# Kernel tuning notes

Hardware: AMD Instinct MI355X
Metric: run time of the kernel (lower is better)

Reference implementation:

```python
import jax, jax.numpy as jnp
import numpy as np

B, T, C = 2, 2048, 1024
H = 4 * C           # MLP hidden (4*n_embd)
E_DYN = 7           # num_experts - static_experts
TOP_K = 2           # num_experts_per_tok
MOE_LOSS_COEF = 0.01


def setup_inputs() -> dict:
    key = jax.random.key(0)
    ks = jax.random.split(key, 6)
    s = 0.02
    x = jax.random.normal(ks[0], (B, T, C), dtype=jnp.float32)
    gate_w = jax.random.normal(ks[1], (C, E_DYN), dtype=jnp.float32) * s
    w1 = jax.random.normal(ks[2], (E_DYN, C, H), dtype=jnp.float32) * s   # dynamic experts c_fc
    w2 = jax.random.normal(ks[3], (E_DYN, H, C), dtype=jnp.float32) * s   # dynamic experts c_proj
    w1s = jax.random.normal(ks[4], (C, H), dtype=jnp.float32) * s         # static expert c_fc
    w2s = jax.random.normal(ks[5], (H, C), dtype=jnp.float32) * s         # static expert c_proj
    return {"x": x, "gate_w": gate_w, "w1": w1, "w2": w2, "w1s": w1s, "w2s": w2s}


def reference(x, gate_w, w1, w2, w1s, w2s):
    b, t, c = x.shape
    xf = x.reshape(-1, c)                                   # [N, C]
    n = xf.shape[0]

    # static expert (always applied)
    y_static = jax.nn.gelu(xf @ w1s, approximate=False) @ w2s  # [N, C]

    # gating: top-k + softmax over selected scores
    scores = xf @ gate_w                                    # [N, E]
    topk_scores, topk_idx = jax.lax.top_k(scores, TOP_K)    # [N, K]
    topk_w = jax.nn.softmax(topk_scores, axis=-1)           # [N, K]

    # dense dispatch weights [N, E] (top_k indices are distinct -> set is safe)
    probs = jnp.zeros((n, E_DYN), dtype=x.dtype)
    probs = probs.at[jnp.arange(n)[:, None], topk_idx].set(topk_w)

    # all-expert MLP then weighted combine (same math as masked per-expert dispatch)
    h = jax.nn.gelu(jnp.einsum('nc,ech->enh', xf, w1), approximate=False)  # [E, N, H]
    y_all = jnp.einsum('enh,ehc->enc', h, w2)               # [E, N, C]
    y_dyn = jnp.einsum('ne,enc->nc', probs, y_all)          # [N, C]

    y = (y_dyn + y_static).reshape(b, t, c)

    # variance_penalty auxiliary loss
    expert_usage = probs.mean(axis=0)                       # [E]
    variance = jnp.mean((expert_usage - expert_usage.mean()) ** 2)
    aux = MOE_LOSS_COEF * variance
    return y, aux
```

## Files before the change

kernel.cpp:

```cpp
#include <hip/hip_runtime.h>
#include <hip/hip_bf16.h>
#include <math.h>

#define N_TOK 4096
#define C_DIM 1024
#define H_DIM 4096
#define NEXP 7
#define NGRP 8
#define HCAP 13184

typedef __attribute__((ext_vector_type(8))) short short8;
typedef __attribute__((ext_vector_type(4))) float floatx4;

static const size_t OFF_COUNTS = 0;
static const size_t OFF_CURSOR = 64;
static const size_t OFF_BASE   = 128;
static const size_t OFF_PCOUNT = 192;
static const size_t OFF_CNT8   = 256;
static const size_t OFF_USAGE  = 320;
static const size_t OFF_TOPKI  = 4096;
static const size_t OFF_TOPKW  = OFF_TOPKI + 8192ull * 4;
static const size_t OFF_ETOK   = OFF_TOPKW + 8192ull * 4;
static const size_t OFF_EWT    = OFF_ETOK + (size_t)HCAP * 4;
static const size_t OFF_EIDX   = OFF_EWT + (size_t)HCAP * 4;
static const size_t OFF_XB     = 262144;
static const size_t OFF_W1T    = OFF_XB + (size_t)N_TOK * C_DIM * 2;
static const size_t OFF_W2T    = OFF_W1T + (size_t)NGRP * H_DIM * C_DIM * 2;
static const size_t OFF_H      = OFF_W2T + (size_t)NGRP * C_DIM * H_DIM * 2;

static __device__ __forceinline__ unsigned short f2bf(float f) {
    __hip_bfloat16 b = __float2bfloat16(f);
    return *reinterpret_cast<unsigned short*>(&b);
}
static __device__ __forceinline__ float bf2f(unsigned short u) {
    unsigned int v = ((unsigned int)u) << 16;
    return __builtin_bit_cast(float, v);
}

static __device__ __forceinline__ float gelu_f(float v) {
    float z = v * 0.70710678118654752f;
    float az = fabsf(z);
    float t = 1.0f / (1.0f + 0.3275911f * az);
    float poly = t * (0.254829592f + t * (-0.284496736f + t * (1.421413741f +
                 t * (-1.453152027f + t * 1.061405429f))));
    float erf_abs = 1.0f - poly * __expf(-az * az);
    float erf_v = (z < 0.f) ? -erf_abs : erf_abs;
    return 0.5f * v * (1.0f + erf_v);
}

static __device__ __forceinline__ void gll16(const void* g, void* l) {
    __builtin_amdgcn_global_load_lds((const __attribute__((address_space(1))) void*)g,
                                     (__attribute__((address_space(3))) void*)l, 16, 0, 0);
}

static __device__ __forceinline__ void wait_vm8() { asm volatile("s_waitcnt vmcnt(8)" ::: "memory"); }
static __device__ __forceinline__ void wait_vm4() { asm volatile("s_waitcnt vmcnt(4)" ::: "memory"); }
static __device__ __forceinline__ void wait_vm0() { asm volatile("s_waitcnt vmcnt(0)" ::: "memory"); }
static __device__ __forceinline__ void barf() {
    __builtin_amdgcn_s_barrier();
    asm volatile("" ::: "memory");
}

__global__ void init_small_kernel(int* counts, int* cursor, float* usage) {
    int i = threadIdx.x;
    if (i < 8) { counts[i] = 0; cursor[i] = 0; usage[i] = 0.f; }
}

__global__ void convert_x_kernel(const float* __restrict__ x, unsigned short* __restrict__ xb) {
    int i = blockIdx.x * 256 + threadIdx.x;
    float4 v = ((const float4*)x)[i];
    ushort4 o;
    o.x = f2bf(v.x); o.y = f2bf(v.y); o.z = f2bf(v.z); o.w = f2bf(v.w);
    ((ushort4*)xb)[i] = o;
}

__global__ __launch_bounds__(256) void transpose_cvt_kernel(
    const float* __restrict__ dyn, const float* __restrict__ stat,
    __hip_bfloat16* __restrict__ dst, int R, int S)
{
    int e = blockIdx.z;
    const float* src = (e < NEXP) ? (dyn + (size_t)e * R * S) : stat;
    unsigned short* d = (unsigned short*)(dst + (size_t)e * R * S);
    int s0 = blockIdx.x * 32, r0 = blockIdx.y * 64;
    __shared__ float t[64][33];
    int tx4 = threadIdx.x & 15, ty4 = threadIdx.x >> 4;
#pragma unroll
    for (int i = 0; i < 4; i++) {
        int r = ty4 + i * 16;
        float2 v = *(const float2*)(src + (size_t)(r0 + r) * S + s0 + tx4 * 2);
        t[r][tx4 * 2] = v.x; t[r][tx4 * 2 + 1] = v.y;
    }
    __syncthreads();
    int tx3 = threadIdx.x & 31, ty3 = threadIdx.x >> 5;
#pragma unroll
    for (int i = 0; i < 4; i++) {
        int s = ty3 + i * 8;
        int r = tx3 * 2;
        ushort2 o;
        o.x = f2bf(t[r][s]); o.y = f2bf(t[r + 1][s]);
        *(ushort2*)(d + (size_t)(s0 + s) * R + r0 + r) = o;
    }
}

__global__ __launch_bounds__(256) void gate_kernel(
    const float* __restrict__ x, const float* __restrict__ gw,
    int* __restrict__ topki, float* __restrict__ topkw,
    int* counts, float* usage)
{
    int wid = threadIdx.x >> 6, lane = threadIdx.x & 63;
    int t = blockIdx.x * 4 + wid;
    float s[NEXP];
#pragma unroll
    for (int e = 0; e < NEXP; e++) s[e] = 0.f;
    for (int c = lane; c < C_DIM; c += 64) {
        float xv = x[(size_t)t * C_DIM + c];
#pragma unroll
        for (int e = 0; e < NEXP; e++) s[e] += xv * gw[c * NEXP + e];
    }
#pragma unroll
    for (int e = 0; e < NEXP; e++)
        for (int off = 32; off > 0; off >>= 1) s[e] += __shfl_xor(s[e], off);
    if (lane == 0) {
        int e0 = 0;
        for (int e = 1; e < NEXP; e++) if (s[e] > s[e0]) e0 = e;
        int e1 = -1;
        for (int e = 0; e < NEXP; e++) {
            if (e == e0) continue;
            if (e1 < 0 || s[e] > s[e1]) e1 = e;
        }
        float w0 = 1.f / (1.f + expf(s[e1] - s[e0]));
        float w1 = 1.f - w0;
        topki[t * 2] = e0; topki[t * 2 + 1] = e1;
        topkw[t * 2] = w0; topkw[t * 2 + 1] = w1;
        atomicAdd(&counts[e0], 1); atomicAdd(&counts[e1], 1);
        atomicAdd(&usage[e0], w0); atomicAdd(&usage[e1], w1);
    }
}

__global__ __launch_bounds__(256) void prefix_kernel(
    const int* counts, const float* usage,
    int* base, int* pcount, int* cnt8,
    int* etok, float* ewt, float* y, int aux_index)
{
    __shared__ int sb[NGRP], sc[NGRP], sp[NGRP];
    if (threadIdx.x == 0) {
        int run = 0;
        for (int g = 0; g < NEXP; g++) {
            int c = counts[g];
            int p = (c + 127) & ~127;
            base[g] = run; pcount[g] = p; cnt8[g] = c;
            sb[g] = run; sc[g] = c; sp[g] = p;
            run += p;
        }
        base[NEXP] = run; pcount[NEXP] = N_TOK; cnt8[NEXP] = N_TOK;
        sb[NEXP] = run; sc[NEXP] = N_TOK; sp[NEXP] = N_TOK;
        float u[NEXP]; float mean = 0.f;
        for (int e = 0; e < NEXP; e++) { u[e] = usage[e] / (float)N_TOK; mean += u[e]; }
        mean /= (float)NEXP;
        float var = 0.f;
        for (int e = 0; e < NEXP; e++) { float dd = u[e] - mean; var += dd * dd; }
        var /= (float)NEXP;
        y[aux_index] = 0.01f * var;
    }
    __syncthreads();
    for (int i = threadIdx.x; i < N_TOK; i += 256) {
        etok[sb[NEXP] + i] = i; ewt[sb[NEXP] + i] = 1.0f;
    }
    for (int g = 0; g < NEXP; g++) {
        for (int i = sc[g] + (int)threadIdx.x; i < sp[g]; i += 256) {
            etok[sb[g] + i] = 0; ewt[sb[g] + i] = 0.f;
        }
    }
}

__global__ void scatter_kernel(const int* __restrict__ topki, const float* __restrict__ topkw,
                               const int* __restrict__ base, int* cursor,
                               int* __restrict__ etok, float* __restrict__ ewt,
                               int* __restrict__ eidx)
{
    int i = blockIdx.x * 256 + threadIdx.x;
    int t = i >> 1;
    int e = topki[i];
    float w = topkw[i];
    int pos = atomicAdd(&cursor[e], 1);
    int idx = base[e] + pos;
    etok[idx] = t; ewt[idx] = w;
    eidx[i] = idx;
}


#define STG1(T) do { int b_ = (T) & 3; size_t so_ = (size_t)(T) * 64; \
        gll16(pA0 + so_, &Als[b_][w * 1024]); \
        gll16(pA1 + so_, &Als[b_][8192 + w * 1024]); \
        gll16(pB0 + so_, &Bls[b_][w * 1024]); \
        gll16(pB1 + so_, &Bls[b_][8192 + w * 1024]); } while (0)

__global__ __launch_bounds__(512, 2) void gemm1_kernel(
    const __hip_bfloat16* __restrict__ xb,
    const __hip_bfloat16* __restrict__ w1t,
    __hip_bfloat16* __restrict__ h,
    const int* __restrict__ etok,
    const int* __restrict__ base,
    const int* __restrict__ pcount)
{
    int id = blockIdx.x;
    int xcd = id & 7, rest = id >> 3;
    int ct = rest & 15, s = rest >> 4;
    int g = s & 7;
    int mt = ((xcd - g) & 7) + 8 * (s >> 3);
    int psz = pcount[g];
    if (mt * 256 >= psz) return;
    int eb = base[g];

    __shared__ __align__(16) char Als[4][16384];
    __shared__ __align__(16) char Bls[4][16384];

    int tid = threadIdx.x, lane = tid & 63, w = tid >> 6;
    int r0 = tid >> 2, c0 = tid & 3;
    int cs = c0 ^ ((r0 >> 1) & 3);

    int tokA0 = etok[eb + mt * 256 + r0];
    int tokA1 = etok[eb + mt * 256 + 128 + r0];
    const char* pA0 = (const char*)(xb + (size_t)tokA0 * C_DIM) + cs * 16;
    const char* pA1 = (const char*)(xb + (size_t)tokA1 * C_DIM) + cs * 16;
    const char* pB0 = (const char*)(w1t + ((size_t)g * H_DIM + ct * 256 + r0) * C_DIM) + cs * 16;
    const char* pB1 = (const char*)(w1t + ((size_t)g * H_DIM + ct * 256 + 128 + r0) * C_DIM) + cs * 16;

    int wm = w >> 2, wn = w & 3;
    int quad = lane >> 4, l16 = lane & 15;
    int rswz = (quad ^ ((l16 >> 1) & 3)) * 16;

    floatx4 acc[8][4] = {};
    const int NT = C_DIM / 32;
    STG1(0); STG1(1); STG1(2);
    for (int T = 0; T < NT; ++T) {
        int rem = NT - 1 - T;
        if (rem >= 2) wait_vm8(); else if (rem == 1) wait_vm4(); else wait_vm0();
        barf();
        if (T + 3 < NT) STG1(T + 3);
        const char* Ap = Als[T & 3];
        const char* Bp = Bls[T & 3];
        short8 a[8], b[4];
#pragma unroll
        for (int i = 0; i < 8; i++)
            a[i] = *(const short8*)(Ap + (wm * 128 + i * 16 + l16) * 64 + rswz);
#pragma unroll
        for (int j = 0; j < 4; j++)
            b[j] = *(const short8*)(Bp + (wn * 64 + j * 16 + l16) * 64 + rswz);
        __builtin_amdgcn_s_setprio(1);
#pragma unroll
        for (int i = 0; i < 8; i++)
#pragma unroll
            for (int j = 0; j < 4; j++)
                acc[i][j] = __builtin_amdgcn_mfma_f32_16x16x32_bf16(a[i], b[j], acc[i][j], 0, 0, 0);
        __builtin_amdgcn_s_setprio(0);
    }

#pragma unroll
    for (int i = 0; i < 8; i++) {
        int lr0 = mt * 256 + wm * 128 + i * 16 + quad * 4;
#pragma unroll
        for (int reg = 0; reg < 4; reg++) {
            int lr = lr0 + reg;
            if (lr < psz) {
                size_t hrow = (size_t)(eb + lr) * H_DIM;
#pragma unroll
                for (int j = 0; j < 4; j++) {
                    int cc = ct * 256 + wn * 64 + j * 16 + l16;
                    h[hrow + cc] = __float2bfloat16(gelu_f(acc[i][j][reg]));
                }
            }
        }
    }
}

__global__ __launch_bounds__(512, 2) void gemm2_kernel(
    const __hip_bfloat16* __restrict__ h,
    const __hip_bfloat16* __restrict__ w2t,
    unsigned short* __restrict__ yp,
    const int* __restrict__ base,
    const int* __restrict__ pcount)
{
    int id = blockIdx.x;
    int xcd = id & 7, rest = id >> 3;
    int ct = rest & 3, s = rest >> 2;
    int g = s & 7;
    int mt = ((xcd - g) & 7) + 8 * (s >> 3);
    int psz = pcount[g];
    if (mt * 256 >= psz) return;
    int eb = base[g];

    __shared__ __align__(16) char Als[4][16384];
    __shared__ __align__(16) char Bls[4][16384];

    int tid = threadIdx.x, lane = tid & 63, w = tid >> 6;
    int r0 = tid >> 2, c0 = tid & 3;
    int cs = c0 ^ ((r0 >> 1) & 3);

    const char* pA0 = (const char*)(h + (size_t)(eb + mt * 256 + r0) * H_DIM) + cs * 16;
    const char* pA1 = (const char*)(h + (size_t)(eb + mt * 256 + 128 + r0) * H_DIM) + cs * 16;
    const char* pB0 = (const char*)(w2t + ((size_t)g * C_DIM + ct * 256 + r0) * H_DIM) + cs * 16;
    const char* pB1 = (const char*)(w2t + ((size_t)g * C_DIM + ct * 256 + 128 + r0) * H_DIM) + cs * 16;

    int wm = w >> 2, wn = w & 3;
    int quad = lane >> 4, l16 = lane & 15;
    int rswz = (quad ^ ((l16 >> 1) & 3)) * 16;

    floatx4 acc[8][4] = {};
    const int NT = H_DIM / 32;
    STG1(0); STG1(1); STG1(2);
    for (int T = 0; T < NT; ++T) {
        int rem = NT - 1 - T;
        if (rem >= 2) wait_vm8(); else if (rem == 1) wait_vm4(); else wait_vm0();
        barf();
        if (T + 3 < NT) STG1(T + 3);
        const char* Ap = Als[T & 3];
        const char* Bp = Bls[T & 3];
        short8 a[8], b[4];
#pragma unroll
        for (int i = 0; i < 8; i++)
            a[i] = *(const short8*)(Ap + (wm * 128 + i * 16 + l16) * 64 + rswz);
#pragma unroll
        for (int j = 0; j < 4; j++)
            b[j] = *(const short8*)(Bp + (wn * 64 + j * 16 + l16) * 64 + rswz);
        __builtin_amdgcn_s_setprio(1);
#pragma unroll
        for (int i = 0; i < 8; i++)
#pragma unroll
            for (int j = 0; j < 4; j++)
                acc[i][j] = __builtin_amdgcn_mfma_f32_16x16x32_bf16(a[i], b[j], acc[i][j], 0, 0, 0);
        __builtin_amdgcn_s_setprio(0);
    }

#pragma unroll
    for (int i = 0; i < 8; i++) {
        int lr0 = mt * 256 + wm * 128 + i * 16 + quad * 4;
#pragma unroll
        for (int reg = 0; reg < 4; reg++) {
            int lr = lr0 + reg;
            if (lr < psz) {
                size_t yrow = (size_t)(eb + lr) * C_DIM;
#pragma unroll
                for (int j = 0; j < 4; j++) {
                    int cc = ct * 256 + wn * 64 + j * 16 + l16;
                    yp[yrow + cc] = f2bf(acc[i][j][reg]);
                }
            }
        }
    }
}

__global__ __launch_bounds__(256) void combine_kernel(
    const unsigned short* __restrict__ yp,
    const int* __restrict__ eidx,
    const float* __restrict__ topkw,
    const int* __restrict__ base,
    float* __restrict__ y)
{
    int t = blockIdx.x;
    int i0 = eidx[t * 2], i1 = eidx[t * 2 + 1];
    float w0 = topkw[t * 2], w1 = topkw[t * 2 + 1];
    int is = base[NEXP] + t;
    int c = threadIdx.x * 4;
    ushort4 a = *(const ushort4*)(yp + (size_t)i0 * C_DIM + c);
    ushort4 b = *(const ushort4*)(yp + (size_t)i1 * C_DIM + c);
    ushort4 s = *(const ushort4*)(yp + (size_t)is * C_DIM + c);
    float4 o;
    o.x = w0 * bf2f(a.x) + w1 * bf2f(b.x) + bf2f(s.x);
    o.y = w0 * bf2f(a.y) + w1 * bf2f(b.y) + bf2f(s.y);
    o.z = w0 * bf2f(a.z) + w1 * bf2f(b.z) + bf2f(s.z);
    o.w = w0 * bf2f(a.w) + w1 * bf2f(b.w) + bf2f(s.w);
    *(float4*)(y + (size_t)t * C_DIM + c) = o;
}

extern "C" void kernel_launch(void* const* d_in, const int* in_sizes, int n_in,
                              void* d_out, int out_size, void* d_ws, size_t ws_size,
                              hipStream_t stream) {
    const float* x      = (const float*)d_in[0];
    const float* gate_w = (const float*)d_in[1];
    const float* w1     = (const float*)d_in[2];
    const float* w2     = (const float*)d_in[3];
    const float* w1s    = (const float*)d_in[4];
    const float* w2s    = (const float*)d_in[5];
    float* y = (float*)d_out;
    char* ws = (char*)d_ws;

    int*   counts = (int*)(ws + OFF_COUNTS);
    int*   cursor = (int*)(ws + OFF_CURSOR);
    int*   base   = (int*)(ws + OFF_BASE);
    int*   pcount = (int*)(ws + OFF_PCOUNT);
    int*   cnt8   = (int*)(ws + OFF_CNT8);
    float* usage  = (float*)(ws + OFF_USAGE);
    int*   topki  = (int*)(ws + OFF_TOPKI);
    float* topkw  = (float*)(ws + OFF_TOPKW);
    int*   etok   = (int*)(ws + OFF_ETOK);
    float* ewt    = (float*)(ws + OFF_EWT);
    int*   eidx   = (int*)(ws + OFF_EIDX);
    unsigned short* xb_u = (unsigned short*)(ws + OFF_XB);
    __hip_bfloat16* xb  = (__hip_bfloat16*)(ws + OFF_XB);
    __hip_bfloat16* w1t = (__hip_bfloat16*)(ws + OFF_W1T);
    __hip_bfloat16* w2t = (__hip_bfloat16*)(ws + OFF_W2T);
    __hip_bfloat16* hbuf = (__hip_bfloat16*)(ws + OFF_H);
    unsigned short* yp  = (unsigned short*)(ws + OFF_W1T);

    init_small_kernel<<<1, 64, 0, stream>>>(counts, cursor, usage);

    convert_x_kernel<<<(N_TOK * C_DIM / 4) / 256, 256, 0, stream>>>(x, xb_u);
    transpose_cvt_kernel<<<dim3(H_DIM / 32, C_DIM / 64, NGRP), 256, 0, stream>>>(w1, w1s, w1t, C_DIM, H_DIM);
    transpose_cvt_kernel<<<dim3(C_DIM / 32, H_DIM / 64, NGRP), 256, 0, stream>>>(w2, w2s, w2t, H_DIM, C_DIM);

    gate_kernel<<<N_TOK / 4, 256, 0, stream>>>(x, gate_w, topki, topkw, counts, usage);
    prefix_kernel<<<1, 256, 0, stream>>>(counts, usage, base, pcount, cnt8, etok, ewt, y, N_TOK * C_DIM);
    scatter_kernel<<<(N_TOK * 2) / 256, 256, 0, stream>>>(topki, topkw, base, cursor, etok, ewt, eidx);

    gemm1_kernel<<<4096, 512, 0, stream>>>(xb, w1t, hbuf, etok, base, pcount);
    gemm2_kernel<<<1024, 512, 0, stream>>>(hbuf, w2t, yp, base, pcount);
    combine_kernel<<<N_TOK, 256, 0, stream>>>(yp, eidx, topkw, base, y);
}
```

Measured before the change: 856.6 us.

## Rewrite grouped GEMM main loop with K=64 double-buffered ping-pong schedule

Replaces the per-K32 four-stage GEMM loop in both expert GEMMs with a shared core that stages K=64 tiles into 128KB of double-buffered LDS. It splits each tile into four quarter MFMA phases with interleaved LDS reads and global-to-LDS prefetches, separated by barriers. It also fuses the x-to-bf16 conversion into the gate kernel and widens the weight transpose tiles to 64x64 with float4 loads. The aim is to hide global latency behind MFMA work and cut kernel launches and memory passes. The cost is more barriers per iteration and a large LDS footprint that may limit occupancy under launch_bounds(512,2).

```diff
diff --git a/kernel.cpp b/kernel.cpp
--- a/kernel.cpp
+++ b/kernel.cpp
@@ -53,27 +53,20 @@
                                      (__attribute__((address_space(3))) void*)l, 16, 0, 0);
 }
 
-static __device__ __forceinline__ void wait_vm8() { asm volatile("s_waitcnt vmcnt(8)" ::: "memory"); }
-static __device__ __forceinline__ void wait_vm4() { asm volatile("s_waitcnt vmcnt(4)" ::: "memory"); }
-static __device__ __forceinline__ void wait_vm0() { asm volatile("s_waitcnt vmcnt(0)" ::: "memory"); }
 static __device__ __forceinline__ void barf() {
     __builtin_amdgcn_s_barrier();
     asm volatile("" ::: "memory");
 }
+static __device__ __forceinline__ void lgkm0s() {
+    asm volatile("s_waitcnt lgkmcnt(0)" ::: "memory");
+    __builtin_amdgcn_sched_barrier(0);
+}
 
 __global__ void init_small_kernel(int* counts, int* cursor, float* usage) {
     int i = threadIdx.x;
     if (i < 8) { counts[i] = 0; cursor[i] = 0; usage[i] = 0.f; }
 }
 
-__global__ void convert_x_kernel(const float* __restrict__ x, unsigned short* __restrict__ xb) {
-    int i = blockIdx.x * 256 + threadIdx.x;
-    float4 v = ((const float4*)x)[i];
-    ushort4 o;
-    o.x = f2bf(v.x); o.y = f2bf(v.y); o.z = f2bf(v.z); o.w = f2bf(v.w);
-    ((ushort4*)xb)[i] = o;
-}
-
 __global__ __launch_bounds__(256) void transpose_cvt_kernel(
     const float* __restrict__ dyn, const float* __restrict__ stat,
     __hip_bfloat16* __restrict__ dst, int R, int S)
@@ -81,29 +74,29 @@
     int e = blockIdx.z;
     const float* src = (e < NEXP) ? (dyn + (size_t)e * R * S) : stat;
     unsigned short* d = (unsigned short*)(dst + (size_t)e * R * S);
-    int s0 = blockIdx.x * 32, r0 = blockIdx.y * 64;
-    __shared__ float t[64][33];
-    int tx4 = threadIdx.x & 15, ty4 = threadIdx.x >> 4;
+    int s0 = blockIdx.x * 64, r0 = blockIdx.y * 64;
+    __shared__ float t[64][65];
+    int lx = (threadIdx.x & 15) * 4, ty = threadIdx.x >> 4;
 #pragma unroll
     for (int i = 0; i < 4; i++) {
-        int r = ty4 + i * 16;
-        float2 v = *(const float2*)(src + (size_t)(r0 + r) * S + s0 + tx4 * 2);
-        t[r][tx4 * 2] = v.x; t[r][tx4 * 2 + 1] = v.y;
+        int r = ty + i * 16;
+        float4 v = *(const float4*)(src + (size_t)(r0 + r) * S + s0 + lx);
+        t[r][lx] = v.x; t[r][lx + 1] = v.y; t[r][lx + 2] = v.z; t[r][lx + 3] = v.w;
     }
     __syncthreads();
-    int tx3 = threadIdx.x & 31, ty3 = threadIdx.x >> 5;
 #pragma unroll
     for (int i = 0; i < 4; i++) {
-        int s = ty3 + i * 8;
-        int r = tx3 * 2;
-        ushort2 o;
-        o.x = f2bf(t[r][s]); o.y = f2bf(t[r + 1][s]);
-        *(ushort2*)(d + (size_t)(s0 + s) * R + r0 + r) = o;
+        int ss = ty + i * 16;
+        ushort4 o;
+        o.x = f2bf(t[lx][ss]); o.y = f2bf(t[lx + 1][ss]);
+        o.z = f2bf(t[lx + 2][ss]); o.w = f2bf(t[lx + 3][ss]);
+        *(ushort4*)(d + (size_t)(s0 + ss) * R + r0 + lx) = o;
     }
 }
 
 __global__ __launch_bounds__(256) void gate_kernel(
     const float* __restrict__ x, const float* __restrict__ gw,
+    unsigned short* __restrict__ xb,
     int* __restrict__ topki, float* __restrict__ topkw,
     int* counts, float* usage)
 {
@@ -112,10 +105,22 @@
     float s[NEXP];
 #pragma unroll
     for (int e = 0; e < NEXP; e++) s[e] = 0.f;
-    for (int c = lane; c < C_DIM; c += 64) {
-        float xv = x[(size_t)t * C_DIM + c];
-#pragma unroll
-        for (int e = 0; e < NEXP; e++) s[e] += xv * gw[c * NEXP + e];
+#pragma unroll
+    for (int it = 0; it < 4; ++it) {
+        int c = it * 256 + lane * 4;
+        float4 xv = *(const float4*)(x + (size_t)t * C_DIM + c);
+        ushort4 o;
+        o.x = f2bf(xv.x); o.y = f2bf(xv.y); o.z = f2bf(xv.z); o.w = f2bf(xv.w);
+        *(ushort4*)(xb + (size_t)t * C_DIM + c) = o;
+        const float* g0 = gw + (size_t)c * NEXP;
+#pragma unroll
+        for (int e = 0; e < NEXP; e++) s[e] += xv.x * g0[e];
+#pragma unroll
+        for (int e = 0; e < NEXP; e++) s[e] += xv.y * g0[NEXP + e];
+#pragma unroll
+        for (int e = 0; e < NEXP; e++) s[e] += xv.z * g0[2 * NEXP + e];
+#pragma unroll
+        for (int e = 0; e < NEXP; e++) s[e] += xv.w * g0[3 * NEXP + e];
     }
 #pragma unroll
     for (int e = 0; e < NEXP; e++)
@@ -189,11 +194,91 @@
 }
 
 
-#define STG1(T) do { int b_ = (T) & 3; size_t so_ = (size_t)(T) * 64; \
-        gll16(pA0 + so_, &Als[b_][w * 1024]); \
-        gll16(pA1 + so_, &Als[b_][8192 + w * 1024]); \
-        gll16(pB0 + so_, &Bls[b_][w * 1024]); \
-        gll16(pB1 + so_, &Bls[b_][8192 + w * 1024]); } while (0)
+static __device__ __forceinline__ void mfma16(const short8 (&a)[8], const short8 (&b)[4],
+                                              floatx4 (&acc)[8][4], int mo, int no) {
+#pragma unroll
+    for (int i = 0; i < 4; i++)
+#pragma unroll
+        for (int j = 0; j < 2; j++)
+#pragma unroll
+            for (int kk = 0; kk < 2; kk++)
+                acc[mo + i][no + j] = __builtin_amdgcn_mfma_f32_16x16x32_bf16(
+                    a[i * 2 + kk], b[j * 2 + kk], acc[mo + i][no + j], 0, 0, 0);
+}
+static __device__ __forceinline__ void rdA(short8 (&d)[8], const char* b, int sw0, int sw1) {
+#pragma unroll
+    for (int i = 0; i < 4; i++) {
+        d[i * 2]     = *(const short8*)(b + i * 2048 + sw0);
+        d[i * 2 + 1] = *(const short8*)(b + i * 2048 + sw1);
+    }
+}
+static __device__ __forceinline__ void rdB(short8 (&d)[4], const char* b, int sw0, int sw1) {
+#pragma unroll
+    for (int j = 0; j < 2; j++) {
+        d[j * 2]     = *(const short8*)(b + j * 2048 + sw0);
+        d[j * 2 + 1] = *(const short8*)(b + j * 2048 + sw1);
+    }
+}
+
+static __device__ __forceinline__ void gemm_core(char* lds, int NKT,
+    const char* pA0, const char* pA1, const char* pA2, const char* pA3,
+    const char* pB0, const char* pB1, const char* pB2, const char* pB3,
+    floatx4 (&acc)[8][4])
+{
+    int tid = threadIdx.x, lane = tid & 63, w = tid >> 6;
+    int wm = w >> 2, wn = w & 3, l16 = lane & 15, quad = lane >> 4;
+    int sw0 = ((quad ^ (l16 & 7)) << 4);
+    int sw1 = (((4 + quad) ^ (l16 & 7)) << 4);
+    int aoff = (wm * 64 + l16) * 128;
+    int boff = (wn * 32 + l16) * 128;
+    int wb = w * 1024;
+    short8 aM0[8], aM1[8], bN0[4], bN1[4];
+
+#define SA_(h, doff, ko) do { \
+    gll16(((h) ? pA1 : pA0) + (ko), lds + (doff) + (h) * 16384 + wb); \
+    gll16(((h) ? pA3 : pA2) + (ko), lds + (doff) + (h) * 16384 + 8192 + wb); } while (0)
+#define SB_(nh, doff, ko) do { \
+    gll16(((nh) ? pB1 : pB0) + (ko), lds + 65536 + (doff) + (nh) * 16384 + wb); \
+    gll16(((nh) ? pB3 : pB2) + (ko), lds + 65536 + (doff) + (nh) * 16384 + 8192 + wb); } while (0)
+
+    SA_(0, 0, 0); SA_(1, 0, 0); SB_(0, 0, 0); SB_(1, 0, 0);
+    SA_(0, 32768, 128); SA_(1, 32768, 128); SB_(0, 32768, 128);
+    asm volatile("s_waitcnt vmcnt(6)" ::: "memory");
+    barf();
+
+#pragma unroll 1
+    for (int T = 0; T < NKT; ++T) {
+        int curo = (T & 1) << 15;
+        int nxto = curo ^ 32768;
+        bool st1 = (T + 1 < NKT), st2 = (T + 2 < NKT);
+        rdA(aM0, lds + curo + aoff, sw0, sw1);
+        rdB(bN0, lds + 65536 + curo + boff, sw0, sw1);
+        if (st1) SB_(1, nxto, 128);
+        barf(); lgkm0s();
+        __builtin_amdgcn_s_setprio(1); mfma16(aM0, bN0, acc, 0, 0); __builtin_amdgcn_s_setprio(0);
+        barf();
+        rdA(aM1, lds + curo + 16384 + aoff, sw0, sw1);
+        if (st2) SA_(0, curo, 256);
+        barf(); lgkm0s();
+        __builtin_amdgcn_s_setprio(1); mfma16(aM1, bN0, acc, 4, 0); __builtin_amdgcn_s_setprio(0);
+        barf();
+        rdB(bN1, lds + 65536 + curo + 16384 + boff, sw0, sw1);
+        if (st2) SA_(1, curo, 256);
+        barf(); lgkm0s();
+        __builtin_amdgcn_s_setprio(1); mfma16(aM0, bN1, acc, 0, 2); __builtin_amdgcn_s_setprio(0);
+        barf();
+        if (st2) SB_(0, curo, 256);
+        barf();
+        __builtin_amdgcn_s_setprio(1); mfma16(aM1, bN1, acc, 4, 2); __builtin_amdgcn_s_setprio(0);
+        if (T >= NKT - 2) { asm volatile("s_waitcnt vmcnt(0)" ::: "memory"); }
+        else              { asm volatile("s_waitcnt vmcnt(6)" ::: "memory"); }
+        barf();
+        pA0 += 128; pA1 += 128; pA2 += 128; pA3 += 128;
+        pB0 += 128; pB1 += 128; pB2 += 128; pB3 += 128;
+    }
+#undef SA_
+#undef SB_
+}
 
 __global__ __launch_bounds__(512, 2) void gemm1_kernel(
     const __hip_bfloat16* __restrict__ xb,
@@ -212,50 +297,30 @@
     if (mt * 256 >= psz) return;
     int eb = base[g];
 
-    __shared__ __align__(16) char Als[4][16384];
-    __shared__ __align__(16) char Bls[4][16384];
+    __shared__ __align__(16) char lds[131072];
 
     int tid = threadIdx.x, lane = tid & 63, w = tid >> 6;
-    int r0 = tid >> 2, c0 = tid & 3;
-    int cs = c0 ^ ((r0 >> 1) & 3);
-
-    int tokA0 = etok[eb + mt * 256 + r0];
-    int tokA1 = etok[eb + mt * 256 + 128 + r0];
-    const char* pA0 = (const char*)(xb + (size_t)tokA0 * C_DIM) + cs * 16;
-    const char* pA1 = (const char*)(xb + (size_t)tokA1 * C_DIM) + cs * 16;
-    const char* pB0 = (const char*)(w1t + ((size_t)g * H_DIM + ct * 256 + r0) * C_DIM) + cs * 16;
-    const char* pB1 = (const char*)(w1t + ((size_t)g * H_DIM + ct * 256 + 128 + r0) * C_DIM) + cs * 16;
-
-    int wm = w >> 2, wn = w & 3;
-    int quad = lane >> 4, l16 = lane & 15;
-    int rswz = (quad ^ ((l16 >> 1) & 3)) * 16;
+    int u0 = 8 * w + (lane >> 3);
+    int v  = (u0 & 31) + ((u0 >> 5) << 6);
+    int ssw = ((lane & 7) ^ (lane >> 3)) * 16;
+
+    int t0 = etok[eb + mt * 256 + u0];
+    int t1 = etok[eb + mt * 256 + 64 + u0];
+    int t2 = etok[eb + mt * 256 + 128 + u0];
+    int t3 = etok[eb + mt * 256 + 192 + u0];
+    const char* pA0 = (const char*)(xb + (size_t)t0 * C_DIM) + ssw;
+    const char* pA1 = (const char*)(xb + (size_t)t1 * C_DIM) + ssw;
+    const char* pA2 = (const char*)(xb + (size_t)t2 * C_DIM) + ssw;
+    const char* pA3 = (const char*)(xb + (size_t)t3 * C_DIM) + ssw;
+    const char* pB0 = (const char*)(w1t + ((size_t)g * H_DIM + ct * 256 + v) * C_DIM) + ssw;
+    const char* pB1 = (const char*)(w1t + ((size_t)g * H_DIM + ct * 256 + v + 32) * C_DIM) + ssw;
+    const char* pB2 = (const char*)(w1t + ((size_t)g * H_DIM + ct * 256 + v + 128) * C_DIM) + ssw;
+    const char* pB3 = (const char*)(w1t + ((size_t)g * H_DIM + ct * 256 + v + 160) * C_DIM) + ssw;
 
     floatx4 acc[8][4] = {};
-    const int NT = C_DIM / 32;
-    STG1(0); STG1(1); STG1(2);
-    for (int T = 0; T < NT; ++T) {
-        int rem = NT - 1 - T;
-        if (rem >= 2) wait_vm8(); else if (rem == 1) wait_vm4(); else wait_vm0();
-        barf();
-        if (T + 3 < NT) STG1(T + 3);
-        const char* Ap = Als[T & 3];
-        const char* Bp = Bls[T & 3];
-        short8 a[8], b[4];
-#pragma unroll
-        for (int i = 0; i < 8; i++)
-            a[i] = *(const short8*)(Ap + (wm * 128 + i * 16 + l16) * 64 + rswz);
-#pragma unroll
-        for (int j = 0; j < 4; j++)
-            b[j] = *(const short8*)(Bp + (wn * 64 + j * 16 + l16) * 64 + rswz);
-        __builtin_amdgcn_s_setprio(1);
-#pragma unroll
-        for (int i = 0; i < 8; i++)
-#pragma unroll
-            for (int j = 0; j < 4; j++)
-                acc[i][j] = __builtin_amdgcn_mfma_f32_16x16x32_bf16(a[i], b[j], acc[i][j], 0, 0, 0);
-        __builtin_amdgcn_s_setprio(0);
-    }
-
+    gemm_core(lds, C_DIM / 64, pA0, pA1, pA2, pA3, pB0, pB1, pB2, pB3, acc);
+
+    int wm = w >> 2, wn = w & 3, l16 = lane & 15, quad = lane >> 4;
 #pragma unroll
     for (int i = 0; i < 8; i++) {
         int lr0 = mt * 256 + wm * 128 + i * 16 + quad * 4;
@@ -290,48 +355,26 @@
     if (mt * 256 >= psz) return;
     int eb = base[g];
 
-    __shared__ __align__(16) char Als[4][16384];
-    __shared__ __align__(16) char Bls[4][16384];
+    __shared__ __align__(16) char lds[131072];
 
     int tid = threadIdx.x, lane = tid & 63, w = tid >> 6;
-    int r0 = tid >> 2, c0 = tid & 3;
-    int cs = c0 ^ ((r0 >> 1) & 3);
-
-    const char* pA0 = (const char*)(h + (size_t)(eb + mt * 256 + r0) * H_DIM) + cs * 16;
-    const char* pA1 = (const char*)(h + (size_t)(eb + mt * 256 + 128 + r0) * H_DIM) + cs * 16;
-    const char* pB0 = (const char*)(w2t + ((size_t)g * C_DIM + ct * 256 + r0) * H_DIM) + cs * 16;
-    const char* pB1 = (const char*)(w2t + ((size_t)g * C_DIM + ct * 256 + 128 + r0) * H_DIM) + cs * 16;
-
-    int wm = w >> 2, wn = w & 3;
-    int quad = lane >> 4, l16 = lane & 15;
-    int rswz = (quad ^ ((l16 >> 1) & 3)) * 16;
+    int u0 = 8 * w + (lane >> 3);
+    int v  = (u0 & 31) + ((u0 >> 5) << 6);
+    int ssw = ((lane & 7) ^ (lane >> 3)) * 16;
+
+    const char* pA0 = (const char*)(h + (size_t)(eb + mt * 256 + u0) * H_DIM) + ssw;
+    const char* pA1 = (const char*)(h + (size_t)(eb + mt * 256 + 64 + u0) * H_DIM) + ssw;
+    const char* pA2 = (const char*)(h + (size_t)(eb + mt * 256 + 128 + u0) * H_DIM) + ssw;
+    const char* pA3 = (const char*)(h + (size_t)(eb + mt * 256 + 192 + u0) * H_DIM) + ssw;
+    const char* pB0 = (const char*)(w2t + ((size_t)g * C_DIM + ct * 256 + v) * H_DIM) + ssw;
+    const char* pB1 = (const char*)(w2t + ((size_t)g * C_DIM + ct * 256 + v + 32) * H_DIM) + ssw;
+    const char* pB2 = (const char*)(w2t + ((size_t)g * C_DIM + ct * 256 + v + 128) * H_DIM) + ssw;
+    const char* pB3 = (const char*)(w2t + ((size_t)g * C_DIM + ct * 256 + v + 160) * H_DIM) + ssw;
 
     floatx4 acc[8][4] = {};
-    const int NT = H_DIM / 32;
-    STG1(0); STG1(1); STG1(2);
-    for (int T = 0; T < NT; ++T) {
-        int rem = NT - 1 - T;
-        if (rem >= 2) wait_vm8(); else if (rem == 1) wait_vm4(); else wait_vm0();
-        barf();
-        if (T + 3 < NT) STG1(T + 3);
-        const char* Ap = Als[T & 3];
-        const char* Bp = Bls[T & 3];
-        short8 a[8], b[4];
-#pragma unroll
-        for (int i = 0; i < 8; i++)
-            a[i] = *(const short8*)(Ap + (wm * 128 + i * 16 + l16) * 64 + rswz);
-#pragma unroll
-        for (int j = 0; j < 4; j++)
-            b[j] = *(const short8*)(Bp + (wn * 64 + j * 16 + l16) * 64 + rswz);
-        __builtin_amdgcn_s_setprio(1);
-#pragma unroll
-        for (int i = 0; i < 8; i++)
-#pragma unroll
-            for (int j = 0; j < 4; j++)
-                acc[i][j] = __builtin_amdgcn_mfma_f32_16x16x32_bf16(a[i], b[j], acc[i][j], 0, 0, 0);
-        __builtin_amdgcn_s_setprio(0);
-    }
-
+    gemm_core(lds, H_DIM / 64, pA0, pA1, pA2, pA3, pB0, pB1, pB2, pB3, acc);
+
+    int wm = w >> 2, wn = w & 3, l16 = lane & 15, quad = lane >> 4;
 #pragma unroll
     for (int i = 0; i < 8; i++) {
         int lr0 = mt * 256 + wm * 128 + i * 16 + quad * 4;
@@ -405,11 +448,10 @@
 
     init_small_kernel<<<1, 64, 0, stream>>>(counts, cursor, usage);
 
-    convert_x_kernel<<<(N_TOK * C_DIM / 4) / 256, 256, 0, stream>>>(x, xb_u);
-    transpose_cvt_kernel<<<dim3(H_DIM / 32, C_DIM / 64, NGRP), 256, 0, stream>>>(w1, w1s, w1t, C_DIM, H_DIM);
-    transpose_cvt_kernel<<<dim3(C_DIM / 32, H_DIM / 64, NGRP), 256, 0, stream>>>(w2, w2s, w2t, H_DIM, C_DIM);
-
-    gate_kernel<<<N_TOK / 4, 256, 0, stream>>>(x, gate_w, topki, topkw, counts, usage);
+    transpose_cvt_kernel<<<dim3(H_DIM / 64, C_DIM / 64, NGRP), 256, 0, stream>>>(w1, w1s, w1t, C_DIM, H_DIM);
+    transpose_cvt_kernel<<<dim3(C_DIM / 64, H_DIM / 64, NGRP), 256, 0, stream>>>(w2, w2s, w2t, H_DIM, C_DIM);
+
+    gate_kernel<<<N_TOK / 4, 256, 0, stream>>>(x, gate_w, xb_u, topki, topkw, counts, usage);
     prefix_kernel<<<1, 256, 0, stream>>>(counts, usage, base, pcount, cnt8, etok, ewt, y, N_TOK * C_DIM);
     scatter_kernel<<<(N_TOK * 2) / 256, 256, 0, stream>>>(topki, topkw, base, cursor, etok, ewt, eidx);
 
```

After: 726.7 us. 15.2% less time.
